# Kernel tuning notes

Measured on AMD Instinct MI355X. Metric: run time of the kernel, lower is better.

The kernel has to match this reference:

```python
import jax, jax.numpy as jnp
import numpy as np
import math

N_HEADS = 16
N_KV_HEADS = 4
D_HEAD = 128
EPS = 1e-6
THETA = 10000.0


def _rmsnorm(x, w):
    var = jnp.mean(x * x, axis=-1, keepdims=True)
    return x * jax.lax.rsqrt(var + EPS) * w


def _rope_tables(S, dtype):
    freqs = 1.0 / THETA ** (jnp.arange(0, D_HEAD, 2, dtype=jnp.float32) / D_HEAD)
    angles = jnp.arange(S, dtype=jnp.float32)[:, None] * freqs[None, :]  # [S, D_HEAD/2]
    angles = jnp.concatenate([angles, angles], axis=-1)  # [S, D_HEAD]
    return jnp.cos(angles).astype(dtype), jnp.sin(angles).astype(dtype)


def _apply_rope(x, cos, sin):
    # x: [B, H, S, D]; rotate-half convention matching cat([angles, angles])
    half = D_HEAD // 2
    x1, x2 = x[..., :half], x[..., half:]
    rot = jnp.concatenate([-x2, x1], axis=-1)
    return x * cos[None, None] + rot * sin[None, None]


def setup_inputs() -> dict:
    key = jax.random.key(0)
    ks = jax.random.split(key, 5)
    B, S, D = 2, 2048, 2048
    s = 0.02
    return {
        "x": jax.random.normal(ks[0], (B, S, D), jnp.float32),
        "Wq": jax.random.normal(ks[1], (D, N_HEADS * D_HEAD), jnp.float32) * s,
        "Wk": jax.random.normal(ks[2], (D, N_KV_HEADS * D_HEAD), jnp.float32) * s,
        "Wv": jax.random.normal(ks[3], (D, N_KV_HEADS * D_HEAD), jnp.float32) * s,
        "Wo": jax.random.normal(ks[4], (D, D), jnp.float32) * s,
        "q_norm_w": jnp.ones((D_HEAD,), jnp.float32),
        "k_norm_w": jnp.ones((D_HEAD,), jnp.float32),
    }


def reference(x, Wq, Wk, Wv, Wo, q_norm_w, k_norm_w):
    B, S, D = x.shape
    groups = N_HEADS // N_KV_HEADS

    q = (x @ Wq).reshape(B, S, N_HEADS, D_HEAD).transpose(0, 2, 1, 3)      # [B,H,S,d]
    k = (x @ Wk).reshape(B, S, N_KV_HEADS, D_HEAD).transpose(0, 2, 1, 3)   # [B,Hkv,S,d]
    v = (x @ Wv).reshape(B, S, N_KV_HEADS, D_HEAD).transpose(0, 2, 1, 3)

    q = _rmsnorm(q, q_norm_w)
    k = _rmsnorm(k, k_norm_w)

    cos, sin = _rope_tables(S, x.dtype)
    q = _apply_rope(q, cos, sin)
    k = _apply_rope(k, cos, sin)

    # GQA broadcast: repeat kv heads into query head dim
    k = jnp.repeat(k, groups, axis=1)  # [B,H,S,d]
    v = jnp.repeat(v, groups, axis=1)

    scale = 1.0 / math.sqrt(D_HEAD)
    scores = jnp.einsum("bhqd,bhkd->bhqk", q, k) * scale
    causal = jnp.tril(jnp.ones((S, S), bool))
    scores = jnp.where(causal[None, None], scores, jnp.finfo(scores.dtype).min)
    probs = jax.nn.softmax(scores, axis=-1)
    out = jnp.einsum("bhqk,bhkd->bhqd", probs, v)  # [B,H,S,d]
    out = out.transpose(0, 2, 1, 3).reshape(B, S, D)
    return out @ Wo
```

## Files before the change

### kernel.cpp

```cpp
#include <hip/hip_runtime.h>
#include <stdint.h>

typedef __attribute__((ext_vector_type(8))) short bf16x8;
typedef __attribute__((ext_vector_type(4))) float f32x4;
typedef __attribute__((ext_vector_type(16))) float f32x16;
typedef unsigned short u16;
typedef unsigned int   u32;
typedef unsigned long long u64;

#define S_LEN 2048
#define NH    16
#define NKV   4
#define DH    128
#define DM    2048
#define QKV_N 3072
#define MROWS 4096

__device__ __forceinline__ u16 f2bf(float x) {
  u32 u = __float_as_uint(x);
  return (u16)((u + 0x7fffu + ((u >> 16) & 1u)) >> 16);
}
__device__ __forceinline__ float bf2f(u16 h) {
  return __uint_as_float(((u32)h) << 16);
}
__device__ __forceinline__ u32 cvtpk(float lo, float hi) {
  u32 r;
  asm("v_cvt_pk_bf16_f32 %0, %1, %2" : "=v"(r) : "v"(lo), "v"(hi));
  return r;
}
__device__ __forceinline__ void plswap(u32& a, u32& b) {
  asm volatile("v_permlane32_swap_b32 %0, %1" : "+v"(a), "+v"(b));
}
__device__ __forceinline__ void gload_lds16(const void* g, void* l) {
  __builtin_amdgcn_global_load_lds((const __attribute__((address_space(1))) void*)g,
                                   (__attribute__((address_space(3))) void*)l, 16, 0, 0);
}

__global__ void __launch_bounds__(256) convert_x_kernel(const float* __restrict__ x,
                                                        u16* __restrict__ o) {
  int idx = (blockIdx.x * 256 + threadIdx.x) * 8;
  float4 a = *(const float4*)(x + idx);
  float4 b = *(const float4*)(x + idx + 4);
  union { u16 s[8]; uint4 v; } t;
  t.s[0] = f2bf(a.x); t.s[1] = f2bf(a.y); t.s[2] = f2bf(a.z); t.s[3] = f2bf(a.w);
  t.s[4] = f2bf(b.x); t.s[5] = f2bf(b.y); t.s[6] = f2bf(b.z); t.s[7] = f2bf(b.w);
  *(uint4*)(o + idx) = t.v;
}

__global__ void __launch_bounds__(256) transpose_all_kernel(const float* __restrict__ Wq,
                                                            const float* __restrict__ Wk,
                                                            const float* __restrict__ Wv,
                                                            const float* __restrict__ Wo,
                                                            u16* __restrict__ wqkvt,
                                                            u16* __restrict__ wot) {
  const int z = blockIdx.z;
  const float* src = (z == 0) ? Wq : (z == 1) ? Wk : (z == 2) ? Wv : Wo;
  u16* dst = (z == 0) ? wqkvt
           : (z == 1) ? (wqkvt + (size_t)2048 * 2048)
           : (z == 2) ? (wqkvt + (size_t)2560 * 2048)
           : wot;
  const int N = (z == 1 || z == 2) ? 512 : 2048;
  if (blockIdx.y * 64 >= N) return;
  __shared__ float t[64][65];
  const int bx = blockIdx.x, by = blockIdx.y, tid = threadIdx.x;
#pragma unroll
  for (int rep = 0; rep < 16; ++rep) {
    int lin = rep * 256 + tid;
    int i = lin >> 6, jj = lin & 63;
    t[i][jj] = src[(size_t)(bx * 64 + i) * N + by * 64 + jj];
  }
  __syncthreads();
#pragma unroll
  for (int rep = 0; rep < 16; ++rep) {
    int lin = rep * 256 + tid;
    int nr = lin >> 6, kc = lin & 63;
    dst[(size_t)(by * 64 + nr) * DM + bx * 64 + kc] = f2bf(t[kc][nr]);
  }
}

__global__ void __launch_bounds__(256) rope_tables_kernel(float* __restrict__ ct,
                                                          float* __restrict__ st_) {
  int idx = blockIdx.x * 256 + threadIdx.x;
  int s = idx >> 6, i = idx & 63;
  const float L2_10000 = 13.287712379549449f;
  float freq = exp2f(-(float)i * (1.0f / 64.0f) * L2_10000);
  float ang = (float)s * freq;
  ct[idx] = cosf(ang);
  st_[idx] = sinf(ang);
}

template <int OUTF32>
__global__ void __launch_bounds__(256) gemm_bt(const u16* __restrict__ A,
                                               const u16* __restrict__ Bt,
                                               void* __restrict__ C,
                                               int M, int N, int K) {
  __shared__ __align__(16) u16 As[128 * 64];
  __shared__ __align__(16) u16 Bs[128 * 64];
  const int tid = threadIdx.x;
  const int w = tid >> 6, l = tid & 63;
  const int g = l >> 4, q15 = l & 15;

  const int nwg = gridDim.x * gridDim.y;
  int bid = blockIdx.y * gridDim.x + blockIdx.x;
  {
    int q = nwg >> 3, r = nwg & 7;
    int xcd = bid & 7, idx = bid >> 3;
    bid = (xcd < r ? xcd * (q + 1) : r * (q + 1) + (xcd - r) * q) + idx;
  }
  const int bx = bid % gridDim.x, by = bid / gridDim.x;
  const int row0 = by * 128, col0 = bx * 128;
  const int wm = (w >> 1) * 64, wn = (w & 1) * 64;
  const f32x4 fz = {0.f, 0.f, 0.f, 0.f};
  f32x4 acc[4][4];
#pragma unroll
  for (int m = 0; m < 4; ++m)
#pragma unroll
    for (int n = 0; n < 4; ++n) acc[m][n] = fz;

  for (int kt = 0; kt < K; kt += 64) {
#pragma unroll
    for (int rnd = 0; rnd < 4; ++rnd) {
      int Pl = rnd * 4096 + tid * 16;
      int arow = Pl >> 7, off = Pl & 127;
      int scol = off ^ ((arow & 7) << 4);
      gload_lds16((const char*)A + ((size_t)(row0 + arow) * K + kt) * 2 + scol,
                  (char*)As + Pl);
      gload_lds16((const char*)Bt + ((size_t)(col0 + arow) * K + kt) * 2 + scol,
                  (char*)Bs + Pl);
    }
    __syncthreads();
#pragma unroll
    for (int kk = 0; kk < 2; ++kk) {
      bf16x8 af[4], bfv[4];
#pragma unroll
      for (int m = 0; m < 4; ++m) {
        int row = wm + m * 16 + q15;
        af[m] = *(const bf16x8*)((const char*)As + row * 128
                                 + ((kk * 64 + g * 16) ^ ((row & 7) << 4)));
      }
#pragma unroll
      for (int n = 0; n < 4; ++n) {
        int row = wn + n * 16 + q15;
        bfv[n] = *(const bf16x8*)((const char*)Bs + row * 128
                                  + ((kk * 64 + g * 16) ^ ((row & 7) << 4)));
      }
#pragma unroll
      for (int m = 0; m < 4; ++m)
#pragma unroll
        for (int n = 0; n < 4; ++n)
          acc[m][n] = __builtin_amdgcn_mfma_f32_16x16x32_bf16(af[m], bfv[n], acc[m][n], 0, 0, 0);
    }
    __syncthreads();
  }
#pragma unroll
  for (int m = 0; m < 4; ++m)
#pragma unroll
    for (int n = 0; n < 4; ++n)
#pragma unroll
      for (int r = 0; r < 4; ++r) {
        int rr = row0 + wm + m * 16 + g * 4 + r;
        int cc = col0 + wn + n * 16 + q15;
        float v = acc[m][n][r];
        if (OUTF32) ((float*)C)[(size_t)rr * N + cc] = v;
        else        ((u16*)C)[(size_t)rr * N + cc]  = f2bf(v);
      }
}

__global__ void __launch_bounds__(256) norm_rope_kernel(const u16* __restrict__ qkv,
                                                        const float* __restrict__ qw,
                                                        const float* __restrict__ kw,
                                                        const float* __restrict__ ct,
                                                        const float* __restrict__ st_,
                                                        u16* __restrict__ Qo,
                                                        u16* __restrict__ Ko) {
  int wid = blockIdx.x * 4 + (threadIdx.x >> 6);
  int l = threadIdx.x & 63;
  int row = wid / 20;
  int j = wid - row * 20;
  int b = row >> 11, s = row & 2047;
  bool isq = j < 16;
  int h = isq ? j : (j - 16);
  const u16* src = qkv + (size_t)row * QKV_N + (isq ? h * DH : (2048 + h * DH));
  float x1 = bf2f(src[l]), x2 = bf2f(src[l + 64]);
  float ss = x1 * x1 + x2 * x2;
#pragma unroll
  for (int off = 32; off > 0; off >>= 1) ss += __shfl_xor(ss, off);
  float rn = rsqrtf(ss * (1.0f / 128.0f) + 1e-6f);
  const float* wv = isq ? qw : kw;
  float n1 = x1 * rn * wv[l], n2 = x2 * rn * wv[l + 64];
  float cv = ct[s * 64 + l], sv = st_[s * 64 + l];
  float o1 = n1 * cv - n2 * sv;
  float o2 = n2 * cv + n1 * sv;
  float scale = isq ? 0.08838834764831845f : 1.0f;
  u16* dst = isq ? (Qo + ((size_t)(b * NH + h) * S_LEN + s) * DH)
                 : (Ko + ((size_t)(b * NKV + h) * S_LEN + s) * DH);
  dst[l]      = f2bf(o1 * scale);
  dst[l + 64] = f2bf(o2 * scale);
}

__global__ void __launch_bounds__(256) vtrans_kernel(const u16* __restrict__ qkv,
                                                     u16* __restrict__ vt) {
  __shared__ u16 t[64][65];
  const int st = blockIdx.x, dt = blockIdx.y, bz = blockIdx.z;
  const int tid = threadIdx.x;
#pragma unroll
  for (int rep = 0; rep < 16; ++rep) {
    int lin = rep * 256 + tid;
    int i = lin >> 6, jj = lin & 63;
    t[i][jj] = qkv[(size_t)((bz >> 2) * S_LEN + st * 64 + i) * QKV_N
                   + 2560 + (bz & 3) * DH + dt * 64 + jj];
  }
  __syncthreads();
#pragma unroll
  for (int rep = 0; rep < 16; ++rep) {
    int lin = rep * 256 + tid;
    int dr = lin >> 6, sc = lin & 63;
    vt[((size_t)bz * DH + dt * 64 + dr) * S_LEN + st * 64 + sc] = t[sc][dr];
  }
}

__global__ void __launch_bounds__(256, 2) attn_kernel(const u16* __restrict__ Qg,
                                                      const u16* __restrict__ Kg,
                                                      const u16* __restrict__ Vt,
                                                      u16* __restrict__ O) {
  __shared__ __align__(16) char smem[65536];
  const int tid = threadIdx.x;
  const int w = tid >> 6, l = tid & 63;
  const int q31 = l & 31, hi = l >> 5;
  const int id = blockIdx.x;
  const int grp = id & 7;
  const int mem = (id >> 3) & 3;
  const int tq  = 15 - (id >> 5);
  const int b   = grp >> 2, kvh = grp & 3;
  const int h   = kvh * 4 + mem;
  const int qb  = tq * 128;
  const int nkt = 2 * tq + 1;
  const int qg  = qb + w * 32 + q31;

  bf16x8 qreg[8];
  const u16* Qrow = Qg + ((size_t)(b * NH + h) * S_LEN + qg) * DH;
#pragma unroll
  for (int c = 0; c < 8; ++c)
    qreg[c] = *(const bf16x8*)(Qrow + c * 16 + hi * 8);

  const char* Kbase = (const char*)(Kg + (size_t)(b * NKV + kvh) * S_LEN * DH);
  const char* Vbase = (const char*)(Vt + (size_t)(b * NKV + kvh) * DH * S_LEN);

  auto stage = [&](int buf, int kt) {
    char* Ksb = smem + buf * 32768;
    char* Vsb = Ksb + 16384;
    const char* Kt  = Kbase + (size_t)kt * 64 * 256;
    const char* Vtb = Vbase + (size_t)kt * 128;
#pragma unroll
    for (int i = 0; i < 4; ++i) {
      int off = w * 4096 + i * 1024 + l * 16;
      int row = off >> 8;
      {
        int cb = (off & 255) ^ ((row & 15) << 4);
        gload_lds16(Kt + (size_t)row * 256 + cb, Ksb + off); }
      {
        int qoff = (off & 255) ^ ((row & 15) << 4);
        int d = row * 2 + (qoff >> 7);
        int kvb = qoff & 127;
        gload_lds16(Vtb + (size_t)d * (S_LEN * 2) + kvb, Vsb + off); }
    }
  };

  f32x16 acc[4];
#pragma unroll
  for (int dt = 0; dt < 4; ++dt)
#pragma unroll
    for (int r = 0; r < 16; ++r) acc[dt][r] = 0.f;
  float mrun = -1e30f, lrun = 0.f;

  stage(0, 0);
  __syncthreads();
  int cur = 0;

  for (int kt = 0; kt <= nkt; ++kt) {
    if (kt < nkt) stage(cur ^ 1, kt + 1);
    const char* Ks = smem + cur * 32768;
    const char* Vs = Ks + 16384;

    f32x16 sa[2];
#pragma unroll
    for (int s = 0; s < 2; ++s)
#pragma unroll
      for (int r = 0; r < 16; ++r) sa[s][r] = 0.f;
    __builtin_amdgcn_s_setprio(1);
#pragma unroll
    for (int s = 0; s < 2; ++s) {
      int krow = s * 32 + q31;
      const char* kr = Ks + krow * 256;
      int sw = (krow & 15) << 4;
#pragma unroll
      for (int c = 0; c < 8; ++c) {
        bf16x8 kf = *(const bf16x8*)(kr + ((c * 32 + hi * 16) ^ sw));
        sa[s] = __builtin_amdgcn_mfma_f32_32x32x16_bf16(kf, qreg[c], sa[s], 0, 0, 0);
      }
    }
    __builtin_amdgcn_s_setprio(0);

    const bool domask = (kt * 64 + 63) > (qb + w * 32);
    float tmax = -1e30f;
#pragma unroll
    for (int s = 0; s < 2; ++s)
#pragma unroll
      for (int r = 0; r < 16; ++r) {
        float v = sa[s][r];
        if (domask) {
          int kvg = kt * 64 + s * 32 + (r & 3) + 8 * (r >> 2) + 4 * hi;
          if (kvg > qg) v = -1e30f;
        }
        sa[s][r] = v;
        tmax = fmaxf(tmax, v);
      }
    tmax = fmaxf(tmax, __shfl_xor(tmax, 32));

    const bool defer = __all(tmax <= mrun + 8.0f);
    const float mnew = defer ? mrun : fmaxf(mrun, tmax);

    float tsum = 0.f;
    union { u32 u[4]; bf16x8 v; } pf[4];
#pragma unroll
    for (int s = 0; s < 2; ++s)
#pragma unroll
      for (int kl = 0; kl < 2; ++kl) {
        float e0 = __expf(sa[s][kl * 8 + 0] - mnew);
        float e1 = __expf(sa[s][kl * 8 + 1] - mnew);
        float e2 = __expf(sa[s][kl * 8 + 2] - mnew);
        float e3 = __expf(sa[s][kl * 8 + 3] - mnew);
        float e4 = __expf(sa[s][kl * 8 + 4] - mnew);
        float e5 = __expf(sa[s][kl * 8 + 5] - mnew);
        float e6 = __expf(sa[s][kl * 8 + 6] - mnew);
        float e7 = __expf(sa[s][kl * 8 + 7] - mnew);
        tsum += (e0 + e1) + (e2 + e3) + (e4 + e5) + (e6 + e7);
        u32 A0 = cvtpk(e0, e1), A1 = cvtpk(e2, e3);
        u32 B0 = cvtpk(e4, e5), B1 = cvtpk(e6, e7);
        plswap(A0, B0);
        plswap(A1, B1);
        int ks = s * 2 + kl;
        pf[ks].u[0] = A0; pf[ks].u[1] = A1; pf[ks].u[2] = B0; pf[ks].u[3] = B1;
      }
    tsum += __shfl_xor(tsum, 32);

    if (defer) {
      lrun += tsum;
    } else {
      float alpha = __expf(mrun - mnew);
      lrun = lrun * alpha + tsum;
      mrun = mnew;
#pragma unroll
      for (int dt = 0; dt < 4; ++dt)
#pragma unroll
        for (int r = 0; r < 16; ++r) acc[dt][r] *= alpha;
    }

    __builtin_amdgcn_s_setprio(1);
#pragma unroll
    for (int dt = 0; dt < 4; ++dt) {
      int d = dt * 32 + q31;
      int vrow = d >> 1;
      const char* vr = Vs + vrow * 256;
      int sw = (vrow & 15) << 4;
      int hb = (d & 1) << 7;
#pragma unroll
      for (int ks = 0; ks < 4; ++ks) {
        bf16x8 vf = *(const bf16x8*)(vr + ((hb | (ks * 32 + hi * 16)) ^ sw));
        acc[dt] = __builtin_amdgcn_mfma_f32_32x32x16_bf16(vf, pf[ks].v, acc[dt], 0, 0, 0);
      }
    }
    __builtin_amdgcn_s_setprio(0);

    __syncthreads();
    cur ^= 1;
  }

  const float linv = 1.0f / lrun;
  u16* Obase = O + ((size_t)b * S_LEN + qg) * DM + h * DH;
#pragma unroll
  for (int dt = 0; dt < 4; ++dt)
#pragma unroll
    for (int rg = 0; rg < 4; ++rg) {
      int d0 = dt * 32 + rg * 8 + hi * 4;
      u32 w0 = cvtpk(acc[dt][rg * 4 + 0] * linv, acc[dt][rg * 4 + 1] * linv);
      u32 w1 = cvtpk(acc[dt][rg * 4 + 2] * linv, acc[dt][rg * 4 + 3] * linv);
      u64 vv = (u64)w0 | ((u64)w1 << 32);
      *(u64*)(Obase + d0) = vv;
    }
}

extern "C" void kernel_launch(void* const* d_in, const int* in_sizes, int n_in,
                              void* d_out, int out_size, void* d_ws, size_t ws_size,
                              hipStream_t stream) {
  (void)in_sizes; (void)n_in; (void)out_size; (void)ws_size;
  const float* x  = (const float*)d_in[0];
  const float* Wq = (const float*)d_in[1];
  const float* Wk = (const float*)d_in[2];
  const float* Wv = (const float*)d_in[3];
  const float* Wo = (const float*)d_in[4];
  const float* qw = (const float*)d_in[5];
  const float* kw = (const float*)d_in[6];

  char* ws = (char*)d_ws;
  u16*   xb    = (u16*)(ws + 0);
  u16*   wqkvt = (u16*)(ws + 16777216);
  u16*   wot   = (u16*)(ws + 29360128);
  u16*   qo    = (u16*)(ws + 37748736);
  u16*   ko    = (u16*)(ws + 54525952);
  u16*   vt    = (u16*)(ws + 58720256);
  float* ctab  = (float*)(ws + 62914560);
  float* stab  = (float*)(ws + 63438848);
  u16*   qkvp  = (u16*)d_out;
  u16*   attn  = (u16*)(ws + 0);
  float* outp  = (float*)d_out;

  convert_x_kernel<<<4096, 256, 0, stream>>>(x, xb);
  transpose_all_kernel<<<dim3(32, 32, 4), 256, 0, stream>>>(Wq, Wk, Wv, Wo, wqkvt, wot);
  rope_tables_kernel<<<512, 256, 0, stream>>>(ctab, stab);

  gemm_bt<0><<<dim3(24, 32), 256, 0, stream>>>(xb, wqkvt, qkvp, MROWS, QKV_N, DM);
  norm_rope_kernel<<<20480, 256, 0, stream>>>(qkvp, qw, kw, ctab, stab, qo, ko);
  vtrans_kernel<<<dim3(32, 2, 8), 256, 0, stream>>>(qkvp, vt);
  attn_kernel<<<512, 256, 0, stream>>>(qo, ko, vt, attn);
  gemm_bt<1><<<dim3(16, 32), 256, 0, stream>>>(attn, wot, outp, MROWS, DM, DM);
}
```

Before: 207.1 us.

## Stage K/V tiles through registers with single LDS buffer for higher occupancy

Replaces the double-buffered direct global-to-LDS K/V staging with a single LDS buffer. The next tile is prefetched into registers during compute and written to LDS between two barriers. LDS use is halved and launch bounds are raised to three blocks per CU, so more waves can hide latency. In exchange it adds an extra barrier per iteration, register pressure from the prefetch buffers, and VGPR round-trips for the loads.

New measurement: 356.5 us. +72.2%, slower.

```diff
diff --git a/kernel.cpp b/kernel.cpp
--- a/kernel.cpp
+++ b/kernel.cpp
@@ -219,11 +219,11 @@
   }
 }
 
-__global__ void __launch_bounds__(256, 2) attn_kernel(const u16* __restrict__ Qg,
+__global__ void __launch_bounds__(256, 3) attn_kernel(const u16* __restrict__ Qg,
                                                       const u16* __restrict__ Kg,
                                                       const u16* __restrict__ Vt,
                                                       u16* __restrict__ O) {
-  __shared__ __align__(16) char smem[65536];
+  __shared__ __align__(16) char smem[32768];
   const int tid = threadIdx.x;
   const int w = tid >> 6, l = tid & 63;
   const int q31 = l & 31, hi = l >> 5;
@@ -245,24 +245,29 @@
 
   const char* Kbase = (const char*)(Kg + (size_t)(b * NKV + kvh) * S_LEN * DH);
   const char* Vbase = (const char*)(Vt + (size_t)(b * NKV + kvh) * DH * S_LEN);
-
-  auto stage = [&](int buf, int kt) {
-    char* Ksb = smem + buf * 32768;
-    char* Vsb = Ksb + 16384;
+  char* Ksb = smem;
+  char* Vsb = smem + 16384;
+
+  uint4 kreg[4], vreg[4];
+  auto ldregs = [&](int kt) {
     const char* Kt  = Kbase + (size_t)kt * 64 * 256;
     const char* Vtb = Vbase + (size_t)kt * 128;
 #pragma unroll
     for (int i = 0; i < 4; ++i) {
       int off = w * 4096 + i * 1024 + l * 16;
       int row = off >> 8;
-      {
-        int cb = (off & 255) ^ ((row & 15) << 4);
-        gload_lds16(Kt + (size_t)row * 256 + cb, Ksb + off); }
-      {
-        int qoff = (off & 255) ^ ((row & 15) << 4);
-        int d = row * 2 + (qoff >> 7);
-        int kvb = qoff & 127;
-        gload_lds16(Vtb + (size_t)d * (S_LEN * 2) + kvb, Vsb + off); }
+      int cb = (off & 255) ^ ((row & 15) << 4);
+      kreg[i] = *(const uint4*)(Kt + (size_t)row * 256 + cb);
+      int d = row * 2 + (cb >> 7);
+      vreg[i] = *(const uint4*)(Vtb + (size_t)d * (S_LEN * 2) + (cb & 127));
+    }
+  };
+  auto stregs = [&]() {
+#pragma unroll
+    for (int i = 0; i < 4; ++i) {
+      int off = w * 4096 + i * 1024 + l * 16;
+      *(uint4*)(Ksb + off) = kreg[i];
+      *(uint4*)(Vsb + off) = vreg[i];
     }
   };
 
@@ -273,14 +278,12 @@
     for (int r = 0; r < 16; ++r) acc[dt][r] = 0.f;
   float mrun = -1e30f, lrun = 0.f;
 
-  stage(0, 0);
+  ldregs(0);
+  stregs();
   __syncthreads();
-  int cur = 0;
 
   for (int kt = 0; kt <= nkt; ++kt) {
-    if (kt < nkt) stage(cur ^ 1, kt + 1);
-    const char* Ks = smem + cur * 32768;
-    const char* Vs = Ks + 16384;
+    if (kt < nkt) ldregs(kt + 1);
 
     f32x16 sa[2];
 #pragma unroll
@@ -291,7 +294,7 @@
 #pragma unroll
     for (int s = 0; s < 2; ++s) {
       int krow = s * 32 + q31;
-      const char* kr = Ks + krow * 256;
+      const char* kr = Ksb + krow * 256;
       int sw = (krow & 15) << 4;
 #pragma unroll
       for (int c = 0; c < 8; ++c) {
@@ -361,7 +364,7 @@
     for (int dt = 0; dt < 4; ++dt) {
       int d = dt * 32 + q31;
       int vrow = d >> 1;
-      const char* vr = Vs + vrow * 256;
+      const char* vr = Vsb + vrow * 256;
       int sw = (vrow & 15) << 4;
       int hb = (d & 1) << 7;
 #pragma unroll
@@ -372,8 +375,11 @@
     }
     __builtin_amdgcn_s_setprio(0);
 
-    __syncthreads();
-    cur ^= 1;
+    if (kt < nkt) {
+      __syncthreads();
+      stregs();
+      __syncthreads();
+    }
   }
 
   const float linv = 1.0f / lrun;
```
